# Performance work log

Measured on AMD Instinct MI355X. Metric: run time of the kernel, lower is better.

## Reference

```python
import jax, jax.numpy as jnp
import numpy as np
from jax import lax

B, T, I, H, O = 2048, 512, 1, 64, 1


def setup_inputs() -> dict:
    key = jax.random.key(0)
    ks = jax.random.split(key, 7)
    stdv = 1.0 / np.sqrt(H)
    return {
        "x": jax.random.normal(ks[0], (B, T, I), dtype=jnp.float32),
        "w_ih": jax.random.uniform(ks[1], (4 * H, I), jnp.float32, -stdv, stdv),
        "w_hh": jax.random.uniform(ks[2], (4 * H, H), jnp.float32, -stdv, stdv),
        "b_ih": jax.random.uniform(ks[3], (4 * H,), jnp.float32, -stdv, stdv),
        "b_hh": jax.random.uniform(ks[4], (4 * H,), jnp.float32, -stdv, stdv),
        "w_fc": jax.random.uniform(ks[5], (O, H), jnp.float32, -stdv, stdv),
        "b_fc": jax.random.uniform(ks[6], (O,), jnp.float32, -stdv, stdv),
    }


def reference(x, w_ih, w_hh, b_ih, b_hh, w_fc, b_fc):
    # x: [B, T, I] (batch_first). Precompute input contribution to gates for all t.
    xT = jnp.swapaxes(x, 0, 1)                                  # [T, B, I]
    x_gates = jnp.einsum("tbi,gi->tbg", xT, w_ih) + b_ih + b_hh  # [T, B, 4H]

    def step(carry, xg):
        h, c = carry
        gates = xg + h @ w_hh.T                                  # [B, 4H]
        i, f, g, o = jnp.split(gates, 4, axis=-1)                # PyTorch gate order i,f,g,o
        i = jax.nn.sigmoid(i)
        f = jax.nn.sigmoid(f)
        g = jnp.tanh(g)
        o = jax.nn.sigmoid(o)
        c = f * c + i * g
        h = o * jnp.tanh(c)
        return (h, c), h

    h0 = jnp.zeros((x.shape[0], w_hh.shape[1]), x.dtype)
    c0 = jnp.zeros_like(h0)
    _, hs = lax.scan(step, (h0, c0), x_gates)                    # hs: [T, B, H]
    hs = jnp.swapaxes(hs, 0, 1)                                  # [B, T, H]
    return hs @ w_fc.T + b_fc                                    # [B, T, O]
```

## Files before the change

kernel.cpp:

```cpp
#include <hip/hip_runtime.h>

#define T_STEPS 512
#define HSTR 80
#define XSTRIDE 520
#define OSTRIDE 513
#define NB 8

typedef _Float16 half8v __attribute__((ext_vector_type(8)));
typedef _Float16 half4v __attribute__((ext_vector_type(4)));
typedef float f32x4 __attribute__((ext_vector_type(4)));

#define K1 1.442695041f
#define K2 2.885390082f

__device__ __forceinline__ float ex2(float x) {
#if __has_builtin(__builtin_amdgcn_exp2f)
    return __builtin_amdgcn_exp2f(x);
#else
    return exp2f(x);
#endif
}
__device__ __forceinline__ float rcp_fast(float x) {
#if __has_builtin(__builtin_amdgcn_rcpf)
    return __builtin_amdgcn_rcpf(x);
#else
    return 1.0f / x;
#endif
}

__device__ __forceinline__ float out_dot(half8v a0, half8v a1,
                                         const float* wfc0, const float* wfc1) {
    float s = 0.f;
#pragma unroll
    for (int j = 0; j < 8; ++j) s = fmaf((float)a0[j], wfc0[j], s);
#pragma unroll
    for (int j = 0; j < 8; ++j) s = fmaf((float)a1[j], wfc1[j], s);
    s += __shfl_xor(s, 16);
    s += __shfl_xor(s, 32);
    return s;
}

__global__ __launch_bounds__(256, 1) void lstm_kernel(
    const float* __restrict__ x, const float* __restrict__ w_ih,
    const float* __restrict__ w_hh, const float* __restrict__ b_ih,
    const float* __restrict__ b_hh, const float* __restrict__ w_fc,
    const float* __restrict__ b_fc, float* __restrict__ out)
{
    __shared__ __align__(16) _Float16 hbuf[2][8 * HSTR];
    __shared__ __align__(16) _Float16 xls[NB * XSTRIDE];
    __shared__ __align__(16) float ols[NB * OSTRIDE];

    const int tid  = threadIdx.x;
    const int w    = tid >> 6;
    const int lane = tid & 63;
    const int q    = lane >> 4;
    const int c    = lane & 15;
    const int hq   = q >> 1;
    const int bat0 = 4 * (q & 1) + 2 * hq;
    const int b0   = blockIdx.x * NB;

    for (int i = tid; i < NB * 128; i += 256) {
        int b  = i >> 7;
        int t4 = i & 127;
        float4 v = *(const float4*)(x + (size_t)(b0 + b) * T_STEPS + t4 * 4);
        half4v hv;
        hv[0] = (_Float16)v.x; hv[1] = (_Float16)v.y;
        hv[2] = (_Float16)v.z; hv[3] = (_Float16)v.w;
        *(half4v*)(&xls[b * XSTRIDE + t4 * 4]) = hv;
    }
    for (int i = tid; i < 2 * 8 * HSTR / 2; i += 256) ((int*)hbuf)[i] = 0;

    const float sK[4] = { -K1, -K1, K2, -K1 };
    half8v bfrag[4][2];
    float biasS[4], wihS[4];
#pragma unroll
    for (int n = 0; n < 4; ++n) {
        int g = 64 * n + 16 * w + c;
        biasS[n] = (b_ih[g] + b_hh[g]) * sK[n];
        wihS[n]  = w_ih[g] * sK[n];
#pragma unroll
        for (int kk = 0; kk < 2; ++kk) {
            const float* wp = w_hh + g * 64 + 32 * kk + 8 * q;
            float4 lo  = *(const float4*)(wp);
            float4 hi4 = *(const float4*)(wp + 4);
            half8v f;
            f[0] = (_Float16)(lo.x  * sK[n]); f[1] = (_Float16)(lo.y  * sK[n]);
            f[2] = (_Float16)(lo.z  * sK[n]); f[3] = (_Float16)(lo.w  * sK[n]);
            f[4] = (_Float16)(hi4.x * sK[n]); f[5] = (_Float16)(hi4.y * sK[n]);
            f[6] = (_Float16)(hi4.z * sK[n]); f[7] = (_Float16)(hi4.w * sK[n]);
            bfrag[n][kk] = f;
        }
    }

    float wfc0[8], wfc1[8];
#pragma unroll
    for (int j = 0; j < 8; ++j) { wfc0[j] = w_fc[8 * q + j]; wfc1[j] = w_fc[32 + 8 * q + j]; }
    const float bfc = b_fc[0];

    float cs[2] = {0.f, 0.f};
    const f32x4 zeroq = {0.f, 0.f, 0.f, 0.f};

    __syncthreads();

    half8v sa0 = {}, sa1 = {};

    for (int tq = 0; tq < 128; ++tq) {
        half4v xh0 = *(const half4v*)(&xls[bat0 * XSTRIDE + tq * 4]);
        half4v xh1 = *(const half4v*)(&xls[(bat0 + 1) * XSTRIDE + tq * 4]);

#pragma unroll
        for (int dt = 0; dt < 4; ++dt) {
            const int t  = tq * 4 + dt;
            const int rb = t & 1;
            const _Float16* hrd = hbuf[rb];

            const _Float16* hp = hrd + (c & 7) * HSTR + 8 * q;
            half8v a0 = *(const half8v*)(hp);
            half8v a1 = *(const half8v*)(hp + 32);

            if (dt == w) { sa0 = a0; sa1 = a1; }

            const float xv0 = (float)xh0[dt], xv1 = (float)xh1[dt];
            float xb0[4], xb1[4];
#pragma unroll
            for (int n = 0; n < 4; ++n) {
                xb0[n] = fmaf(xv0, wihS[n], biasS[n]);
                xb1[n] = fmaf(xv1, wihS[n], biasS[n]);
            }

            f32x4 acc[4];
#pragma unroll
            for (int n = 0; n < 4; ++n) {
                acc[n] = __builtin_amdgcn_mfma_f32_16x16x32_f16(a1, bfrag[n][1], zeroq, 0, 0, 0);
                acc[n] = __builtin_amdgcn_mfma_f32_16x16x32_f16(a0, bfrag[n][0], acc[n], 0, 0, 0);
            }

            float v[4][2];
#pragma unroll
            for (int n = 0; n < 4; ++n) {
                v[n][0] = (hq ? acc[n][2] : acc[n][0]) + xb0[n];
                v[n][1] = (hq ? acc[n][3] : acc[n][1]) + xb1[n];
            }

            _Float16* hwr = hbuf[rb ^ 1];
#pragma unroll
            for (int rr = 0; rr < 2; ++rr) {
                float A  = ex2(v[0][rr]);
                float B  = ex2(v[2][rr]);
                float ig = (B - 1.0f) * rcp_fast((1.0f + A) * (1.0f + B));
                float rf = rcp_fast(1.0f + ex2(v[1][rr]));
                cs[rr] = fmaf(cs[rr], rf, ig);
                float cc = fminf(fmaxf(cs[rr], -15.f), 15.f);
                float Ao = ex2(v[3][rr]);
                float C  = ex2(cc * K2);
                float h  = (C - 1.0f) * rcp_fast((1.0f + Ao) * (1.0f + C));
                hwr[(bat0 + rr) * HSTR + 16 * w + c] = (_Float16)h;
            }
            __syncthreads();
        }

        {
            int st = tq * 4 + w;
            if (st > 0) {
                float s = out_dot(sa0, sa1, wfc0, wfc1);
                if (lane < NB) ols[lane * OSTRIDE + (st - 1)] = s + bfc;
            }
        }
    }

    if (w == 3) {
        const _Float16* hp = hbuf[0] + (c & 7) * HSTR + 8 * q;
        half8v a0 = *(const half8v*)(hp);
        half8v a1 = *(const half8v*)(hp + 32);
        float s = out_dot(a0, a1, wfc0, wfc1);
        if (lane < NB) ols[lane * OSTRIDE + (T_STEPS - 1)] = s + bfc;
    }
    __syncthreads();

    for (int i = tid; i < NB * T_STEPS; i += 256) {
        int b = i >> 9;
        int t = i & (T_STEPS - 1);
        out[(size_t)(b0 + b) * T_STEPS + t] = ols[b * OSTRIDE + t];
    }
}

extern "C" void kernel_launch(void* const* d_in, const int* in_sizes, int n_in,
                              void* d_out, int out_size, void* d_ws, size_t ws_size,
                              hipStream_t stream) {
    const float* x    = (const float*)d_in[0];
    const float* w_ih = (const float*)d_in[1];
    const float* w_hh = (const float*)d_in[2];
    const float* b_ih = (const float*)d_in[3];
    const float* b_hh = (const float*)d_in[4];
    const float* w_fc = (const float*)d_in[5];
    const float* b_fc = (const float*)d_in[6];
    float* out = (float*)d_out;
    hipLaunchKernelGGL(lstm_kernel, dim3(2048 / NB), dim3(256), 0, stream,
                       x, w_ih, w_hh, b_ih, b_hh, w_fc, b_fc, out);
}
```

Baseline: 264.8 us.

## Halve batch per block to 4 and run two blocks per CU

Each block now handles 4 batch rows instead of 8, doubling the grid to 512 blocks, and launch bounds allow two blocks per CU. The MFMA A-fragment replicates each batch row across four lanes, so each lane evaluates the gate nonlinearities for one batch row instead of two. This shortens the serial per-step nonlinearity chain and lets two independent recurrences interleave per CU to hide barrier and MFMA latency. The cost is more redundant MFMA work per useful batch row and higher register pressure under the tighter launch bound.

```diff
diff --git a/kernel.cpp b/kernel.cpp
--- a/kernel.cpp
+++ b/kernel.cpp
@@ -4,7 +4,7 @@
 #define HSTR 80
 #define XSTRIDE 520
 #define OSTRIDE 513
-#define NB 8
+#define NB 4
 
 typedef _Float16 half8v __attribute__((ext_vector_type(8)));
 typedef _Float16 half4v __attribute__((ext_vector_type(4)));
@@ -40,13 +40,13 @@
     return s;
 }
 
-__global__ __launch_bounds__(256, 1) void lstm_kernel(
+__global__ __launch_bounds__(256, 2) void lstm_kernel(
     const float* __restrict__ x, const float* __restrict__ w_ih,
     const float* __restrict__ w_hh, const float* __restrict__ b_ih,
     const float* __restrict__ b_hh, const float* __restrict__ w_fc,
     const float* __restrict__ b_fc, float* __restrict__ out)
 {
-    __shared__ __align__(16) _Float16 hbuf[2][8 * HSTR];
+    __shared__ __align__(16) _Float16 hbuf[2][NB * HSTR];
     __shared__ __align__(16) _Float16 xls[NB * XSTRIDE];
     __shared__ __align__(16) float ols[NB * OSTRIDE];
 
@@ -55,8 +55,7 @@
     const int lane = tid & 63;
     const int q    = lane >> 4;
     const int c    = lane & 15;
-    const int hq   = q >> 1;
-    const int bat0 = 4 * (q & 1) + 2 * hq;
+    const int bown = q;
     const int b0   = blockIdx.x * NB;
 
     for (int i = tid; i < NB * 128; i += 256) {
@@ -68,7 +67,7 @@
         hv[2] = (_Float16)v.z; hv[3] = (_Float16)v.w;
         *(half4v*)(&xls[b * XSTRIDE + t4 * 4]) = hv;
     }
-    for (int i = tid; i < 2 * 8 * HSTR / 2; i += 256) ((int*)hbuf)[i] = 0;
+    for (int i = tid; i < 2 * NB * HSTR / 2; i += 256) ((int*)hbuf)[i] = 0;
 
     const float sK[4] = { -K1, -K1, K2, -K1 };
     half8v bfrag[4][2];
@@ -97,7 +96,7 @@
     for (int j = 0; j < 8; ++j) { wfc0[j] = w_fc[8 * q + j]; wfc1[j] = w_fc[32 + 8 * q + j]; }
     const float bfc = b_fc[0];
 
-    float cs[2] = {0.f, 0.f};
+    float cs = 0.f;
     const f32x4 zeroq = {0.f, 0.f, 0.f, 0.f};
 
     __syncthreads();
@@ -105,8 +104,7 @@
     half8v sa0 = {}, sa1 = {};
 
     for (int tq = 0; tq < 128; ++tq) {
-        half4v xh0 = *(const half4v*)(&xls[bat0 * XSTRIDE + tq * 4]);
-        half4v xh1 = *(const half4v*)(&xls[(bat0 + 1) * XSTRIDE + tq * 4]);
+        half4v xh = *(const half4v*)(&xls[bown * XSTRIDE + tq * 4]);
 
 #pragma unroll
         for (int dt = 0; dt < 4; ++dt) {
@@ -114,19 +112,16 @@
             const int rb = t & 1;
             const _Float16* hrd = hbuf[rb];
 
-            const _Float16* hp = hrd + (c & 7) * HSTR + 8 * q;
+            const _Float16* hp = hrd + (c >> 2) * HSTR + 8 * q;
             half8v a0 = *(const half8v*)(hp);
             half8v a1 = *(const half8v*)(hp + 32);
 
             if (dt == w) { sa0 = a0; sa1 = a1; }
 
-            const float xv0 = (float)xh0[dt], xv1 = (float)xh1[dt];
-            float xb0[4], xb1[4];
+            const float xv = (float)xh[dt];
+            float xb[4];
 #pragma unroll
-            for (int n = 0; n < 4; ++n) {
-                xb0[n] = fmaf(xv0, wihS[n], biasS[n]);
-                xb1[n] = fmaf(xv1, wihS[n], biasS[n]);
-            }
+            for (int n = 0; n < 4; ++n) xb[n] = fmaf(xv, wihS[n], biasS[n]);
 
             f32x4 acc[4];
 #pragma unroll
@@ -135,26 +130,22 @@
                 acc[n] = __builtin_amdgcn_mfma_f32_16x16x32_f16(a0, bfrag[n][0], acc[n], 0, 0, 0);
             }
 
-            float v[4][2];
+            float v4[4];
 #pragma unroll
-            for (int n = 0; n < 4; ++n) {
-                v[n][0] = (hq ? acc[n][2] : acc[n][0]) + xb0[n];
-                v[n][1] = (hq ? acc[n][3] : acc[n][1]) + xb1[n];
-            }
+            for (int n = 0; n < 4; ++n) v4[n] = acc[n][0] + xb[n];
 
             _Float16* hwr = hbuf[rb ^ 1];
-#pragma unroll
-            for (int rr = 0; rr < 2; ++rr) {
-                float A  = ex2(v[0][rr]);
-                float B  = ex2(v[2][rr]);
-                float ig = (B - 1.0f) * rcp_fast((1.0f + A) * (1.0f + B));
-                float rf = rcp_fast(1.0f + ex2(v[1][rr]));
-                cs[rr] = fmaf(cs[rr], rf, ig);
-                float cc = fminf(fmaxf(cs[rr], -15.f), 15.f);
-                float Ao = ex2(v[3][rr]);
+            {
+                float A  = ex2(v4[0]);
+                float Bt = ex2(v4[2]);
+                float ig = (Bt - 1.0f) * rcp_fast((1.0f + A) * (1.0f + Bt));
+                float rf = rcp_fast(1.0f + ex2(v4[1]));
+                cs = fmaf(cs, rf, ig);
+                float cc = fminf(fmaxf(cs, -15.f), 15.f);
+                float Ao = ex2(v4[3]);
                 float C  = ex2(cc * K2);
                 float h  = (C - 1.0f) * rcp_fast((1.0f + Ao) * (1.0f + C));
-                hwr[(bat0 + rr) * HSTR + 16 * w + c] = (_Float16)h;
+                hwr[bown * HSTR + 16 * w + c] = (_Float16)h;
             }
             __syncthreads();
         }
@@ -163,17 +154,19 @@
             int st = tq * 4 + w;
             if (st > 0) {
                 float s = out_dot(sa0, sa1, wfc0, wfc1);
-                if (lane < NB) ols[lane * OSTRIDE + (st - 1)] = s + bfc;
+                if (lane < 16 && (lane & 3) == 0)
+                    ols[(lane >> 2) * OSTRIDE + (st - 1)] = s + bfc;
             }
         }
     }
 
     if (w == 3) {
-        const _Float16* hp = hbuf[0] + (c & 7) * HSTR + 8 * q;
+        const _Float16* hp = hbuf[0] + (c >> 2) * HSTR + 8 * q;
         half8v a0 = *(const half8v*)(hp);
         half8v a1 = *(const half8v*)(hp + 32);
         float s = out_dot(a0, a1, wfc0, wfc1);
-        if (lane < NB) ols[lane * OSTRIDE + (T_STEPS - 1)] = s + bfc;
+        if (lane < 16 && (lane & 3) == 0)
+            ols[(lane >> 2) * OSTRIDE + (T_STEPS - 1)] = s + bfc;
     }
     __syncthreads();
 
```

Result: faster. 254.7 us (-3.8%).
